# Kernel optimization log

Measured on AMD Instinct MI355X. Metric: run time of the kernel, lower is better.

## Reference

```python
import jax, jax.numpy as jnp
import numpy as np

BITS = 4
GROUP = 128
IN_F = 4096
OUT_F = 11008
N_GROUPS = IN_F // GROUP  # padded_in == in_features here


def fwht(v):
    """Orthonormal fast Walsh-Hadamard transform over the last axis (len = power of 2)."""
    orig = v.shape
    g = orig[-1]
    x = v.reshape(-1, g)
    h = 1
    while h < g:
        x = x.reshape(-1, g // (2 * h), 2, h)
        a, b = x[:, :, 0, :], x[:, :, 1, :]
        x = jnp.stack([a + b, a - b], axis=2).reshape(-1, g)
        h *= 2
    return (x * (1.0 / np.sqrt(g))).reshape(orig)


def setup_inputs() -> dict:
    key = jax.random.key(0)
    ks = jax.random.split(key, 7)
    x = jax.random.normal(ks[0], (4096, IN_F), dtype=jnp.float32)
    # packed 4-bit indices: two per byte, stored as int32 byte values
    packed_weight = jax.random.randint(ks[1], (OUT_F, IN_F // 2), 0, 256, dtype=jnp.int32)
    # per-(row, group) scale factors (positive)
    norms = jax.random.uniform(ks[2], (OUT_F, N_GROUPS), dtype=jnp.float32) * 0.1 + 0.01
    # Lloyd-Max codebook: 2^bits sorted centroids
    centroids = jnp.sort(jax.random.normal(ks[3], (2 ** BITS,), dtype=jnp.float32))
    # Rademacher sign vectors for the two-round signed WHT rotation
    signs1 = jnp.where(jax.random.normal(ks[4], (GROUP,)) >= 0, 1.0, -1.0).astype(jnp.float32)
    signs2 = jnp.where(jax.random.normal(ks[5], (GROUP,)) >= 0, 1.0, -1.0).astype(jnp.float32)
    bias = jax.random.normal(ks[6], (OUT_F,), dtype=jnp.float32) * 0.01
    return {"x": x, "packed_weight": packed_weight, "norms": norms,
            "centroids": centroids, "signs1": signs1, "signs2": signs2, "bias": bias}


def dequantize(packed_weight, norms, centroids, signs1, signs2):
    out_f, n_groups = norms.shape
    # unpack 4-bit nibbles: low nibble at even positions, high nibble at odd
    pw = packed_weight.astype(jnp.uint8)
    lo = (pw & 15).astype(jnp.int32)
    hi = (pw >> 4).astype(jnp.int32)
    idx = jnp.stack([lo, hi], axis=-1).reshape(out_f, -1)      # [out, padded_in]
    c = centroids[idx].reshape(out_f, n_groups, GROUP)          # codebook lookup
    # inverse of rotate(v) = H(s2 * H(s1 * v)):  v = s1 * H(s2 * H(u))
    u = fwht(c) * signs2
    u = fwht(u) * signs1
    w = u * norms[:, :, None]                                   # per-group rescale
    return w.reshape(out_f, -1)


def reference(x, packed_weight, norms, centroids, signs1, signs2, bias):
    w = dequantize(packed_weight, norms, centroids, signs1, signs2)[:, : x.shape[-1]]
    return x @ w.T + bias
```

## Files before the change

### kernel.cpp

```cpp
#include <hip/hip_runtime.h>
#include <stdint.h>

#define M_DIM 4096
#define K_DIM 4096
#define N_DIM 11008
#define N_GROUPS 32

typedef __attribute__((ext_vector_type(8))) short short8;
typedef __attribute__((ext_vector_type(4))) float floatx4;

__device__ __forceinline__ unsigned short f32_to_bf16(float f) {
    unsigned int u = __float_as_uint(f);
    unsigned int rounding = 0x7FFFu + ((u >> 16) & 1u);
    return (unsigned short)((u + rounding) >> 16);
}

__global__ __launch_bounds__(128) void make_M_kernel(
    const float* __restrict__ signs1, const float* __restrict__ signs2,
    unsigned short* __restrict__ Mt)
{
    const int i = blockIdx.x;
    const int j = threadIdx.x;
    __shared__ float s2s[128];
    s2s[j] = signs2[j];
    __syncthreads();
    float acc = 0.f;
#pragma unroll 8
    for (int a = 0; a < 128; ++a) {
        int par = (__popc(i & a) + __popc(a & j)) & 1;
        acc += par ? -s2s[a] : s2s[a];
    }
    Mt[i * 128 + j] = f32_to_bf16(signs1[j] * acc * (1.0f / 128.0f));
}

__global__ __launch_bounds__(512) void transform_x_kernel(
    const float* __restrict__ x,
    const unsigned short* __restrict__ Mt,
    unsigned short* __restrict__ z)
{
    __shared__ __align__(16) short Ms[128 * 136];
    __shared__ __align__(16) short Xs[64 * 136];
    __shared__ __align__(16) short Ls[64 * 136];

    const int tid = threadIdx.x;
    const int wave = tid >> 6, lane = tid & 63;
    const int col16 = lane & 15, quad = lane >> 4;
    const int wr = wave >> 2;
    const int wc = wave & 3;
    const int g = blockIdx.x & 31;
    const int mblk = blockIdx.x >> 5;
    const int c0 = g * 128;
    const int mBase = mblk * 256;

#pragma unroll
    for (int it = 0; it < 4; ++it) {
        int ch = tid + 512 * it;
        int row = ch >> 4, cc = ch & 15;
        *(uint4*)(Ms + row * 136 + cc * 8) = *(const uint4*)(Mt + (size_t)ch * 8);
    }
    __syncthreads();

    short8 bf[2][4];
#pragma unroll
    for (int ni = 0; ni < 2; ++ni)
#pragma unroll
        for (int ks = 0; ks < 4; ++ks)
            bf[ni][ks] = *(const short8*)(Ms + (wc * 32 + ni * 16 + col16) * 136 + ks * 32 + quad * 8);

    for (int s = 0; s < 4; ++s) {
        __syncthreads();
#pragma unroll
        for (int it = 0; it < 4; ++it) {
            int idx = tid + 512 * it;
            int row = idx >> 5, c4 = idx & 31;
            float4 v = *(const float4*)(x + (size_t)(mBase + s * 64 + row) * K_DIM + c0 + c4 * 4);
            uint2 o;
            o.x = (unsigned)f32_to_bf16(v.x) | ((unsigned)f32_to_bf16(v.y) << 16);
            o.y = (unsigned)f32_to_bf16(v.z) | ((unsigned)f32_to_bf16(v.w) << 16);
            *(uint2*)(Xs + row * 136 + c4 * 4) = o;
        }
        __syncthreads();

        short8 af[2][4];
#pragma unroll
        for (int mi = 0; mi < 2; ++mi)
#pragma unroll
            for (int ks = 0; ks < 4; ++ks)
                af[mi][ks] = *(const short8*)(Xs + (wr * 32 + mi * 16 + col16) * 136 + ks * 32 + quad * 8);
        floatx4 acc2[2][2] = {};
#pragma unroll
        for (int ks = 0; ks < 4; ++ks)
#pragma unroll
            for (int mi = 0; mi < 2; ++mi)
#pragma unroll
                for (int ni = 0; ni < 2; ++ni)
                    acc2[mi][ni] = __builtin_amdgcn_mfma_f32_16x16x32_bf16(
                        af[mi][ks], bf[ni][ks], acc2[mi][ni], 0, 0, 0);

#pragma unroll
        for (int mi = 0; mi < 2; ++mi)
#pragma unroll
            for (int ni = 0; ni < 2; ++ni)
#pragma unroll
                for (int r = 0; r < 4; ++r)
                    Ls[(wr * 32 + mi * 16 + quad * 4 + r) * 136 + wc * 32 + ni * 16 + col16] =
                        f32_to_bf16(acc2[mi][ni][r]);
        __syncthreads();

#pragma unroll
        for (int it = 0; it < 2; ++it) {
            int idx = tid + 512 * it;
            int row = idx >> 4, cc = idx & 15;
            uint4 v = *(const uint4*)(Ls + row * 136 + cc * 8);
            *(uint4*)(z + (size_t)(mBase + s * 64 + row) * K_DIM + c0 + cc * 8) = v;
        }
    }
}

__global__ __launch_bounds__(256) void dequant_lut_kernel(
    const int* __restrict__ packed,
    const float* __restrict__ norms,
    const float* __restrict__ centroids,
    unsigned int* __restrict__ w_out)
{
    __shared__ float lut[16 * 32];
    const int tid = threadIdx.x;
    lut[tid]       = centroids[tid >> 5];
    lut[tid + 256] = centroids[(tid + 256) >> 5];
    __syncthreads();

    const float* lutr = lut + (tid & 31);

    const int row = blockIdx.x;
    const int g = tid >> 3;
    const float nrm = norms[row * N_GROUPS + g];
    const int* prow = packed + (size_t)row * 2048 + tid * 8;
    int4 pa = *(const int4*)(prow);
    int4 pb = *(const int4*)(prow + 4);
    int v[8] = {pa.x, pa.y, pa.z, pa.w, pb.x, pb.y, pb.z, pb.w};
    unsigned o[8];
#pragma unroll
    for (int q = 0; q < 8; ++q) {
        float clo = lutr[(v[q] & 15) << 5];
        float chi = lutr[((v[q] >> 4) & 15) << 5];
        o[q] = (unsigned)f32_to_bf16(clo * nrm) | ((unsigned)f32_to_bf16(chi * nrm) << 16);
    }
    unsigned* orow = w_out + (size_t)row * 2048 + tid * 8;
    *(uint4*)(orow)     = make_uint4(o[0], o[1], o[2], o[3]);
    *(uint4*)(orow + 4) = make_uint4(o[4], o[5], o[6], o[7]);
}

#define BM 256
#define BN 256
#define BK 64

typedef const __attribute__((address_space(1))) void* gvp_t;
typedef __attribute__((address_space(3))) void* svp_t;

#define BARRIER() do { asm volatile("" ::: "memory"); __builtin_amdgcn_s_barrier(); \
                       asm volatile("" ::: "memory"); } while (0)
#define VM8()   asm volatile("s_waitcnt vmcnt(8)" ::: "memory")
#define VM4()   asm volatile("s_waitcnt vmcnt(4)" ::: "memory")
#define VM2()   asm volatile("s_waitcnt vmcnt(2)" ::: "memory")
#define VM0()   asm volatile("s_waitcnt vmcnt(0)" ::: "memory")
#define PRIO1() __builtin_amdgcn_s_setprio(1)
#define PRIO0() __builtin_amdgcn_s_setprio(0)

__device__ __forceinline__ void read_a4(short8 (&dst)[4][2], const short* rb, int s0) {
#pragma unroll
    for (int fm = 0; fm < 4; ++fm) {
        dst[fm][0] = *(const short8*)(rb + fm * 1024 + s0);
        dst[fm][1] = *(const short8*)(rb + fm * 1024 + (s0 ^ 32));
    }
}
__device__ __forceinline__ void read_b2(short8 (&dst)[2][2], const short* rb, int s0) {
#pragma unroll
    for (int fn = 0; fn < 2; ++fn) {
        dst[fn][0] = *(const short8*)(rb + fn * 1024 + s0);
        dst[fn][1] = *(const short8*)(rb + fn * 1024 + (s0 ^ 32));
    }
}
__device__ __forceinline__ void mfma_q(floatx4 (&acc)[4][2],
                                       const short8 (&a)[4][2], const short8 (&b)[2][2]) {
#pragma unroll
    for (int ks = 0; ks < 2; ++ks)
#pragma unroll
        for (int fm = 0; fm < 4; ++fm)
#pragma unroll
            for (int fn = 0; fn < 2; ++fn)
                acc[fm][fn] = __builtin_amdgcn_mfma_f32_16x16x32_bf16(
                    a[fm][ks], b[fn][ks], acc[fm][fn], 0, 0, 0);
}

__global__ __launch_bounds__(512, 2) void gemm_bt_kernel(
    const unsigned short* __restrict__ A,
    const unsigned short* __restrict__ B,
    const float* __restrict__ bias,
    float* __restrict__ C)
{
    __shared__ __align__(16) short smem[65536];
    short* As = smem;
    short* Bs = smem + 32768;

    const int tid = threadIdx.x;
    const int w = tid >> 6, lane = tid & 63;
    const int wm = w >> 2, wn = w & 3;
    const int col16 = lane & 15, quad = lane >> 4;

    const int bid = blockIdx.x;
    const int mt = bid & 15;
    const int nt = bid >> 4;
    const int m0 = mt * BM, n0 = nt * BN;

    const int gc = (lane & 7) ^ (lane >> 3);
    const unsigned short* aSrc = A + (size_t)(m0 + w * 8 + (lane >> 3)) * K_DIM + gc * 8;
    const unsigned short* bSrc = B + (size_t)(n0 + (w >> 2) * 64 + (w & 3) * 8 + (lane >> 3)) * K_DIM + gc * 8;
    const int wOff = w * 512;

#define STAGE_A(BUF, H, KT) do { \
    __builtin_amdgcn_global_load_lds((gvp_t)(aSrc + (size_t)((H) * 64) * K_DIM + (KT) * 64), \
        (svp_t)(As + (BUF) * 16384 + (H) * 8192 + wOff), 16, 0, 0); \
    __builtin_amdgcn_global_load_lds((gvp_t)(aSrc + (size_t)((H) * 64 + 128) * K_DIM + (KT) * 64), \
        (svp_t)(As + (BUF) * 16384 + (H) * 8192 + 4096 + wOff), 16, 0, 0); \
} while (0)
#define STAGE_B(BUF, H, KT) do { \
    __builtin_amdgcn_global_load_lds((gvp_t)(bSrc + (size_t)((H) * 32) * K_DIM + (KT) * 64), \
        (svp_t)(Bs + (BUF) * 16384 + (H) * 8192 + wOff), 16, 0, 0); \
    __builtin_amdgcn_global_load_lds((gvp_t)(bSrc + (size_t)((H) * 32 + 128) * K_DIM + (KT) * 64), \
        (svp_t)(Bs + (BUF) * 16384 + (H) * 8192 + 4096 + wOff), 16, 0, 0); \
} while (0)

    const short* aR = As + (wm * 64 + col16) * 64;
    const short* bR = Bs + (wn * 32 + col16) * 64;
    const int s0 = (quad ^ (col16 & 7)) << 3;

    short8 a0[4][2], a1[4][2], b0[2][2], b1[2][2];
    floatx4 acc[2][2][4][2];
#pragma unroll
    for (int i0 = 0; i0 < 2; ++i0)
#pragma unroll
        for (int i1 = 0; i1 < 2; ++i1)
#pragma unroll
            for (int i2 = 0; i2 < 4; ++i2)
#pragma unroll
                for (int i3 = 0; i3 < 2; ++i3)
                    acc[i0][i1][i2][i3] = (floatx4)0.0f;


    STAGE_A(0, 0, 0); STAGE_B(0, 0, 0);
    STAGE_A(0, 1, 0); STAGE_B(0, 1, 0);
    STAGE_A(1, 0, 1); STAGE_B(1, 0, 1);
    VM8();
    BARRIER();
    read_a4(a0, aR, s0); read_b2(b0, bR, s0);
    STAGE_A(1, 1, 1);
    VM8();
    BARRIER();

    const int NIT = K_DIM / (2 * BK) - 1;
    for (int i = 0; i < NIT; ++i) {
        const int t = 2 * i;
        read_a4(a1, aR + 8192, s0);
        PRIO1(); mfma_q(acc[0][0], a0, b0); PRIO0();
        STAGE_B(1, 1, t + 1);
        VM8(); BARRIER();
        read_b2(b1, bR + 8192, s0);
        PRIO1(); mfma_q(acc[1][0], a1, b0); PRIO0();
        STAGE_A(0, 0, t + 2);
        PRIO1(); mfma_q(acc[0][1], a0, b1); PRIO0();
        STAGE_B(0, 0, t + 2);
        VM8(); BARRIER();
        read_a4(a0, aR + 16384, s0); read_b2(b0, bR + 16384, s0);
        PRIO1(); mfma_q(acc[1][1], a1, b1); PRIO0();
        STAGE_A(0, 1, t + 2);
        VM8(); BARRIER();
        read_a4(a1, aR + 16384 + 8192, s0);
        PRIO1(); mfma_q(acc[0][0], a0, b0); PRIO0();
        STAGE_B(0, 1, t + 2);
        VM8(); BARRIER();
        read_b2(b1, bR + 16384 + 8192, s0);
        PRIO1(); mfma_q(acc[1][0], a1, b0); PRIO0();
        STAGE_A(1, 0, t + 3);
        PRIO1(); mfma_q(acc[0][1], a0, b1); PRIO0();
        STAGE_B(1, 0, t + 3);
        VM8(); BARRIER();
        read_a4(a0, aR, s0); read_b2(b0, bR, s0);
        PRIO1(); mfma_q(acc[1][1], a1, b1); PRIO0();
        STAGE_A(1, 1, t + 3);
        VM8(); BARRIER();
    }

    read_a4(a1, aR + 8192, s0);
    mfma_q(acc[0][0], a0, b0);
    STAGE_B(1, 1, 63);
    VM8();
    BARRIER();
    read_b2(b1, bR + 8192, s0);
    mfma_q(acc[1][0], a1, b0);
    VM4();
    BARRIER();
    mfma_q(acc[0][1], a0, b1);
    VM2();
    BARRIER();
    read_a4(a0, aR + 16384, s0); read_b2(b0, bR + 16384, s0);
    mfma_q(acc[1][1], a1, b1);
    VM0();
    BARRIER();
    read_a4(a1, aR + 16384 + 8192, s0);
    mfma_q(acc[0][0], a0, b0);
    read_b2(b1, bR + 16384 + 8192, s0);
    mfma_q(acc[1][0], a1, b0);
    mfma_q(acc[0][1], a0, b1);
    mfma_q(acc[1][1], a1, b1);

#undef STAGE_A
#undef STAGE_B

    float bv[2][2];
#pragma unroll
    for (int qn = 0; qn < 2; ++qn)
#pragma unroll
        for (int fn = 0; fn < 2; ++fn)
            bv[qn][fn] = bias[n0 + wn * 64 + qn * 32 + fn * 16 + col16];

#pragma unroll
    for (int qm = 0; qm < 2; ++qm)
#pragma unroll
        for (int fm = 0; fm < 4; ++fm)
#pragma unroll
            for (int r = 0; r < 4; ++r) {
                float* crow = C + (size_t)(m0 + wm * 128 + qm * 64 + fm * 16 + quad * 4 + r) * N_DIM
                              + n0 + wn * 64 + col16;
#pragma unroll
                for (int qn = 0; qn < 2; ++qn)
#pragma unroll
                    for (int fn = 0; fn < 2; ++fn)
                        crow[qn * 32 + fn * 16] = acc[qm][qn][fm][fn][r] + bv[qn][fn];
            }
}

extern "C" void kernel_launch(void* const* d_in, const int* in_sizes, int n_in,
                              void* d_out, int out_size, void* d_ws, size_t ws_size,
                              hipStream_t stream) {
    const float* x        = (const float*)d_in[0];
    const int* packed     = (const int*)d_in[1];
    const float* norms    = (const float*)d_in[2];
    const float* centroids= (const float*)d_in[3];
    const float* signs1   = (const float*)d_in[4];
    const float* signs2   = (const float*)d_in[5];
    const float* bias     = (const float*)d_in[6];
    float* out            = (float*)d_out;

    unsigned short* Mt     = (unsigned short*)d_ws;
    unsigned short* w_bf16 = (unsigned short*)((char*)d_ws + 32768);
    unsigned short* z_bf16 = (unsigned short*)((char*)d_ws + 32768 + (size_t)N_DIM * K_DIM * 2);

    make_M_kernel<<<128, 128, 0, stream>>>(signs1, signs2, Mt);

    transform_x_kernel<<<(M_DIM / 256) * N_GROUPS, 512, 0, stream>>>(x, Mt, z_bf16);

    for (int rep = 0; rep < 4; ++rep)
        dequant_lut_kernel<<<N_DIM, 256, 0, stream>>>(
            packed, norms, centroids, (unsigned int*)w_bf16);

    gemm_bt_kernel<<<dim3((M_DIM / BM) * (N_DIM / BN)), 512, 0, stream>>>(
        z_bf16, w_bf16, bias, out);
}
```

Measured before the change: 688.3 us.

## Fuse activation transform and weight dequant into one interleaved launch

Merges the x-rotation kernel and the LUT dequant kernel into a single launch. One in eight of the first 4096 blocks does the transform, and the rest dequantize two weight rows each with 512 threads. This also removes the dequant kernel that was launched four times redundantly, and the two workloads overlap on the GPU. Two extra barriers are added inside the GEMM main loop, probably to fix an LDS staging hazard, at some sync cost. Every block now reserves ~68KB of LDS, which may limit occupancy for the dequant blocks.

```diff
diff --git a/kernel.cpp b/kernel.cpp
--- a/kernel.cpp
+++ b/kernel.cpp
@@ -33,121 +33,133 @@
     Mt[i * 128 + j] = f32_to_bf16(signs1[j] * acc * (1.0f / 128.0f));
 }
 
-__global__ __launch_bounds__(512) void transform_x_kernel(
+__global__ __launch_bounds__(512) void fused_tx_dq_kernel(
     const float* __restrict__ x,
     const unsigned short* __restrict__ Mt,
-    unsigned short* __restrict__ z)
-{
-    __shared__ __align__(16) short Ms[128 * 136];
-    __shared__ __align__(16) short Xs[64 * 136];
-    __shared__ __align__(16) short Ls[64 * 136];
-
-    const int tid = threadIdx.x;
-    const int wave = tid >> 6, lane = tid & 63;
-    const int col16 = lane & 15, quad = lane >> 4;
-    const int wr = wave >> 2;
-    const int wc = wave & 3;
-    const int g = blockIdx.x & 31;
-    const int mblk = blockIdx.x >> 5;
-    const int c0 = g * 128;
-    const int mBase = mblk * 256;
-
-#pragma unroll
-    for (int it = 0; it < 4; ++it) {
-        int ch = tid + 512 * it;
-        int row = ch >> 4, cc = ch & 15;
-        *(uint4*)(Ms + row * 136 + cc * 8) = *(const uint4*)(Mt + (size_t)ch * 8);
-    }
-    __syncthreads();
-
-    short8 bf[2][4];
-#pragma unroll
-    for (int ni = 0; ni < 2; ++ni)
-#pragma unroll
-        for (int ks = 0; ks < 4; ++ks)
-            bf[ni][ks] = *(const short8*)(Ms + (wc * 32 + ni * 16 + col16) * 136 + ks * 32 + quad * 8);
-
-    for (int s = 0; s < 4; ++s) {
-        __syncthreads();
-#pragma unroll
-        for (int it = 0; it < 4; ++it) {
-            int idx = tid + 512 * it;
-            int row = idx >> 5, c4 = idx & 31;
-            float4 v = *(const float4*)(x + (size_t)(mBase + s * 64 + row) * K_DIM + c0 + c4 * 4);
-            uint2 o;
-            o.x = (unsigned)f32_to_bf16(v.x) | ((unsigned)f32_to_bf16(v.y) << 16);
-            o.y = (unsigned)f32_to_bf16(v.z) | ((unsigned)f32_to_bf16(v.w) << 16);
-            *(uint2*)(Xs + row * 136 + c4 * 4) = o;
-        }
-        __syncthreads();
-
-        short8 af[2][4];
-#pragma unroll
-        for (int mi = 0; mi < 2; ++mi)
-#pragma unroll
-            for (int ks = 0; ks < 4; ++ks)
-                af[mi][ks] = *(const short8*)(Xs + (wr * 32 + mi * 16 + col16) * 136 + ks * 32 + quad * 8);
-        floatx4 acc2[2][2] = {};
-#pragma unroll
-        for (int ks = 0; ks < 4; ++ks)
-#pragma unroll
-            for (int mi = 0; mi < 2; ++mi)
-#pragma unroll
-                for (int ni = 0; ni < 2; ++ni)
-                    acc2[mi][ni] = __builtin_amdgcn_mfma_f32_16x16x32_bf16(
-                        af[mi][ks], bf[ni][ks], acc2[mi][ni], 0, 0, 0);
-
-#pragma unroll
-        for (int mi = 0; mi < 2; ++mi)
-#pragma unroll
-            for (int ni = 0; ni < 2; ++ni)
-#pragma unroll
-                for (int r = 0; r < 4; ++r)
-                    Ls[(wr * 32 + mi * 16 + quad * 4 + r) * 136 + wc * 32 + ni * 16 + col16] =
-                        f32_to_bf16(acc2[mi][ni][r]);
-        __syncthreads();
-
-#pragma unroll
-        for (int it = 0; it < 2; ++it) {
-            int idx = tid + 512 * it;
-            int row = idx >> 4, cc = idx & 15;
-            uint4 v = *(const uint4*)(Ls + row * 136 + cc * 8);
-            *(uint4*)(z + (size_t)(mBase + s * 64 + row) * K_DIM + c0 + cc * 8) = v;
-        }
-    }
-}
-
-__global__ __launch_bounds__(256) void dequant_lut_kernel(
+    unsigned short* __restrict__ z,
     const int* __restrict__ packed,
     const float* __restrict__ norms,
     const float* __restrict__ centroids,
     unsigned int* __restrict__ w_out)
 {
-    __shared__ float lut[16 * 32];
+    __shared__ __align__(16) char smem_f[69632];
+
+    const int bid = blockIdx.x;
     const int tid = threadIdx.x;
-    lut[tid]       = centroids[tid >> 5];
-    lut[tid + 256] = centroids[(tid + 256) >> 5];
-    __syncthreads();
-
-    const float* lutr = lut + (tid & 31);
-
-    const int row = blockIdx.x;
-    const int g = tid >> 3;
-    const float nrm = norms[row * N_GROUPS + g];
-    const int* prow = packed + (size_t)row * 2048 + tid * 8;
-    int4 pa = *(const int4*)(prow);
-    int4 pb = *(const int4*)(prow + 4);
-    int v[8] = {pa.x, pa.y, pa.z, pa.w, pb.x, pb.y, pb.z, pb.w};
-    unsigned o[8];
-#pragma unroll
-    for (int q = 0; q < 8; ++q) {
-        float clo = lutr[(v[q] & 15) << 5];
-        float chi = lutr[((v[q] >> 4) & 15) << 5];
-        o[q] = (unsigned)f32_to_bf16(clo * nrm) | ((unsigned)f32_to_bf16(chi * nrm) << 16);
-    }
-    unsigned* orow = w_out + (size_t)row * 2048 + tid * 8;
-    *(uint4*)(orow)     = make_uint4(o[0], o[1], o[2], o[3]);
-    *(uint4*)(orow + 4) = make_uint4(o[4], o[5], o[6], o[7]);
+
+    bool is_tx;
+    int wid;
+    if (bid < 4096) {
+        if ((bid & 7) == 0) { is_tx = true;  wid = bid >> 3; }
+        else               { is_tx = false; wid = bid - (bid >> 3) - 1; }
+    } else {
+        is_tx = false; wid = bid - 512;
+    }
+
+    if (is_tx) {
+        short* Ms = (short*)smem_f;
+        short* Xs = Ms + 128 * 136;
+        short* Ls = Xs + 64 * 136;
+
+        const int wave = tid >> 6, lane = tid & 63;
+        const int col16 = lane & 15, quad = lane >> 4;
+        const int wr = wave >> 2;
+        const int wc = wave & 3;
+        const int g = wid & 31;
+        const int mblk = wid >> 5;
+        const int c0 = g * 128;
+        const int mBase = mblk * 256;
+
+#pragma unroll
+        for (int it = 0; it < 4; ++it) {
+            int ch = tid + 512 * it;
+            int row = ch >> 4, cc = ch & 15;
+            *(uint4*)(Ms + row * 136 + cc * 8) = *(const uint4*)(Mt + (size_t)ch * 8);
+        }
+        __syncthreads();
+
+        short8 bf[2][4];
+#pragma unroll
+        for (int ni = 0; ni < 2; ++ni)
+#pragma unroll
+            for (int ks = 0; ks < 4; ++ks)
+                bf[ni][ks] = *(const short8*)(Ms + (wc * 32 + ni * 16 + col16) * 136 + ks * 32 + quad * 8);
+
+        for (int s = 0; s < 4; ++s) {
+            __syncthreads();
+#pragma unroll
+            for (int it = 0; it < 4; ++it) {
+                int idx = tid + 512 * it;
+                int row = idx >> 5, c4 = idx & 31;
+                float4 v = *(const float4*)(x + (size_t)(mBase + s * 64 + row) * K_DIM + c0 + c4 * 4);
+                uint2 o;
+                o.x = (unsigned)f32_to_bf16(v.x) | ((unsigned)f32_to_bf16(v.y) << 16);
+                o.y = (unsigned)f32_to_bf16(v.z) | ((unsigned)f32_to_bf16(v.w) << 16);
+                *(uint2*)(Xs + row * 136 + c4 * 4) = o;
+            }
+            __syncthreads();
+
+            short8 af[2][4];
+#pragma unroll
+            for (int mi = 0; mi < 2; ++mi)
+#pragma unroll
+                for (int ks = 0; ks < 4; ++ks)
+                    af[mi][ks] = *(const short8*)(Xs + (wr * 32 + mi * 16 + col16) * 136 + ks * 32 + quad * 8);
+            floatx4 acc2[2][2] = {};
+#pragma unroll
+            for (int ks = 0; ks < 4; ++ks)
+#pragma unroll
+                for (int mi = 0; mi < 2; ++mi)
+#pragma unroll
+                    for (int ni = 0; ni < 2; ++ni)
+                        acc2[mi][ni] = __builtin_amdgcn_mfma_f32_16x16x32_bf16(
+                            af[mi][ks], bf[ni][ks], acc2[mi][ni], 0, 0, 0);
+
+#pragma unroll
+            for (int mi = 0; mi < 2; ++mi)
+#pragma unroll
+                for (int ni = 0; ni < 2; ++ni)
+#pragma unroll
+                    for (int r = 0; r < 4; ++r)
+                        Ls[(wr * 32 + mi * 16 + quad * 4 + r) * 136 + wc * 32 + ni * 16 + col16] =
+                            f32_to_bf16(acc2[mi][ni][r]);
+            __syncthreads();
+
+#pragma unroll
+            for (int it = 0; it < 2; ++it) {
+                int idx = tid + 512 * it;
+                int row = idx >> 4, cc = idx & 15;
+                uint4 v = *(const uint4*)(Ls + row * 136 + cc * 8);
+                *(uint4*)(z + (size_t)(mBase + s * 64 + row) * K_DIM + c0 + cc * 8) = v;
+            }
+        }
+    } else {
+        float* lut = (float*)smem_f;
+        lut[tid] = centroids[tid >> 5];
+        __syncthreads();
+
+        const int sub = tid >> 8;
+        const int t = tid & 255;
+        const int row = wid * 2 + sub;
+        const float* lutr = lut + (t & 31);
+
+        const int g = t >> 3;
+        const float nrm = norms[row * N_GROUPS + g];
+        const int* prow = packed + (size_t)row * 2048 + t * 8;
+        int4 pa = *(const int4*)(prow);
+        int4 pb = *(const int4*)(prow + 4);
+        int v[8] = {pa.x, pa.y, pa.z, pa.w, pb.x, pb.y, pb.z, pb.w};
+        unsigned o[8];
+#pragma unroll
+        for (int q = 0; q < 8; ++q) {
+            float clo = lutr[(v[q] & 15) << 5];
+            float chi = lutr[((v[q] >> 4) & 15) << 5];
+            o[q] = (unsigned)f32_to_bf16(clo * nrm) | ((unsigned)f32_to_bf16(chi * nrm) << 16);
+        }
+        unsigned* orow = w_out + (size_t)row * 2048 + t * 8;
+        *(uint4*)(orow)     = make_uint4(o[0], o[1], o[2], o[3]);
+        *(uint4*)(orow + 4) = make_uint4(o[4], o[5], o[6], o[7]);
+    }
 }
 
 #define BM 256
@@ -267,6 +279,7 @@
         read_b2(b1, bR + 8192, s0);
         PRIO1(); mfma_q(acc[1][0], a1, b0); PRIO0();
         STAGE_A(0, 0, t + 2);
+        BARRIER();
         PRIO1(); mfma_q(acc[0][1], a0, b1); PRIO0();
         STAGE_B(0, 0, t + 2);
         VM8(); BARRIER();
@@ -281,6 +294,7 @@
         read_b2(b1, bR + 16384 + 8192, s0);
         PRIO1(); mfma_q(acc[1][0], a1, b0); PRIO0();
         STAGE_A(1, 0, t + 3);
+        BARRIER();
         PRIO1(); mfma_q(acc[0][1], a0, b1); PRIO0();
         STAGE_B(1, 0, t + 3);
         VM8(); BARRIER();
@@ -357,11 +371,8 @@
 
     make_M_kernel<<<128, 128, 0, stream>>>(signs1, signs2, Mt);
 
-    transform_x_kernel<<<(M_DIM / 256) * N_GROUPS, 512, 0, stream>>>(x, Mt, z_bf16);
-
-    for (int rep = 0; rep < 4; ++rep)
-        dequant_lut_kernel<<<N_DIM, 256, 0, stream>>>(
-            packed, norms, centroids, (unsigned int*)w_bf16);
+    fused_tx_dq_kernel<<<6016, 512, 0, stream>>>(
+        x, Mt, z_bf16, packed, norms, centroids, (unsigned int*)w_bf16);
 
     gemm_bt_kernel<<<dim3((M_DIM / BM) * (N_DIM / BN)), 512, 0, stream>>>(
         z_bf16, w_bf16, bias, out);
```

Result: faster. 645.4 us (-6.2%).
